# Performance work log

Hardware: AMD Instinct MI355X
Metric: run time of the kernel (lower is better)

The kernel has to match this reference:

```python
import jax, jax.numpy as jnp
import numpy as np

LN_EPS = 1e-5
NEG_SLOPE = 0.01  # torch LeakyReLU default


def layernorm(x, w, b):
    m = jnp.mean(x, axis=-1, keepdims=True)
    v = jnp.mean((x - m) ** 2, axis=-1, keepdims=True)
    return (x - m) * jax.lax.rsqrt(v + LN_EPS) * w + b


def setup_inputs() -> dict:
    key = jax.random.key(0)
    ks = jax.random.split(key, 12)
    B, T, C, E = 16, 1024, 768, 2
    d = C
    s = 0.02
    inp = {
        "x": jax.random.normal(ks[0], (B, T, C), jnp.float32),
        "ln1_w": jnp.ones((C,), jnp.float32),
        "ln1_b": jnp.zeros((C,), jnp.float32),
        "wqkv": jax.random.normal(ks[1], (C, 3 * C), jnp.float32) * s,
        "bqkv": jnp.zeros((3 * C,), jnp.float32),
        "wproj": jax.random.normal(ks[2], (C, C), jnp.float32) * s,
        "bproj": jnp.zeros((C,), jnp.float32),
        "ln2_w": jnp.ones((C,), jnp.float32),
        "ln2_b": jnp.zeros((C,), jnp.float32),
        "wg": jax.random.normal(ks[3], (C, E), jnp.float32) * s,
        # Experts module uses torch.randn (std 1); we scale down for numerics
        "w1": jax.random.normal(ks[4], (E, d, 4 * d), jnp.float32) * s,
        "w2": jax.random.normal(ks[5], (E, 4 * d, 4 * d), jnp.float32) * s,
        "w3": jax.random.normal(ks[6], (E, 4 * d, d), jnp.float32) * s,
        "n_head": 12,
    }
    return inp


def block_forward(x, ln1_w, ln1_b, wqkv, bqkv, wproj, bproj,
                  ln2_w, ln2_b, wg, w1, w2, w3, n_head):
    B, T, C = x.shape
    H = n_head
    hd = C // H
    E = wg.shape[-1]

    # ---- causal self-attention + residual ----
    h = layernorm(x, ln1_w, ln1_b)
    qkv = h @ wqkv + bqkv                      # [B,T,3C]
    q, k, v = jnp.split(qkv, 3, axis=-1)
    q = q.reshape(B, T, H, hd).transpose(0, 2, 1, 3)  # bhtd
    k = k.reshape(B, T, H, hd).transpose(0, 2, 1, 3)
    v = v.reshape(B, T, H, hd).transpose(0, 2, 1, 3)
    scores = jnp.einsum('bhqd,bhkd->bhqk', q, k) / jnp.sqrt(jnp.float32(hd))
    causal = jnp.tril(jnp.ones((T, T), bool))
    scores = jnp.where(causal, scores, jnp.finfo(scores.dtype).min)
    attn = jax.nn.softmax(scores, axis=-1)
    y = jnp.einsum('bhqk,bhkd->bhqd', attn, v)
    y = y.transpose(0, 2, 1, 3).reshape(B, T, C)
    x = x + (y @ wproj + bproj)

    # ---- MoE (top-2 gating, capacity dispatch) + residual ----
    h2 = layernorm(x, ln2_w, ln2_b)
    capacity = (T * 2) // E                    # capacity_factor = 1.0, top-2
    raw_gates = jax.nn.softmax(h2 @ wg, axis=-1)   # [B,T,E]

    idx1 = jnp.argmax(raw_gates, axis=-1)
    mask1 = jax.nn.one_hot(idx1, E, dtype=raw_gates.dtype)
    gate1 = jnp.sum(raw_gates * mask1, axis=-1)    # [B,T]
    gates2 = raw_gates * (1.0 - mask1)
    idx2 = jnp.argmax(gates2, axis=-1)
    mask2 = jax.nn.one_hot(idx2, E, dtype=raw_gates.dtype)
    gate2 = jnp.sum(raw_gates * mask2, axis=-1)
    denom = gate1 + gate2 + 1e-9
    gate1, gate2 = gate1 / denom, gate2 / denom

    # aux load-balancing loss (before capacity truncation)
    density = jnp.mean(mask1, axis=1)              # [B,E]
    density_proxy = jnp.mean(raw_gates, axis=1)    # [B,E]
    aux_loss = jnp.mean(density * density_proxy) * (E * E)

    # positions within each expert buffer (exclusive cumsum over tokens)
    pos1 = jnp.cumsum(mask1, axis=1) - mask1       # [B,T,E]
    mask1 = mask1 * (pos1 < capacity)
    mask1_count = jnp.sum(mask1, axis=1, keepdims=True)
    pos2 = (jnp.cumsum(mask2, axis=1) - mask2) + mask1_count
    mask2 = mask2 * (pos2 < capacity)

    oh1 = jax.nn.one_hot(pos1.astype(jnp.int32), capacity, dtype=raw_gates.dtype)
    oh2 = jax.nn.one_hot(pos2.astype(jnp.int32), capacity, dtype=raw_gates.dtype)
    combine = (gate1[..., None] * mask1)[..., None] * oh1 \
            + (gate2[..., None] * mask2)[..., None] * oh2   # [B,T,E,C]
    dispatch = (combine > 0).astype(h2.dtype)

    # dispatch -> per-expert batches
    expert_in = jnp.einsum('bnd,bnec->ebcd', h2, dispatch)   # [E,B,Cap,d]
    Bc = B * capacity
    ei = expert_in.reshape(E, Bc, C)
    lrelu = lambda z: jnp.where(z >= 0, z, NEG_SLOPE * z)
    hh = lrelu(jnp.einsum('end,edh->enh', ei, w1))
    hh = lrelu(jnp.einsum('end,edh->enh', hh, w2))
    eo = jnp.einsum('end,edh->enh', hh, w3).reshape(E, B, capacity, C)
    moe_out = jnp.einsum('ebcd,bnec->bnd', eo, combine)

    x = x + moe_out
    return x, aux_loss


def reference(x, ln1_w, ln1_b, wqkv, bqkv, wproj, bproj,
              ln2_w, ln2_b, wg, w1, w2, w3, n_head):
    return block_forward(x, ln1_w, ln1_b, wqkv, bqkv, wproj, bproj,
                         ln2_w, ln2_b, wg, w1, w2, w3, n_head)
```

## Files before the change

### kernel.cpp

```cpp
#include <hip/hip_runtime.h>
#include <cstdint>
#include <cstddef>

constexpr int B_  = 16;
constexpr int T_  = 1024;
constexpr int C_  = 768;
constexpr int H_  = 12;
constexpr int HD_ = 64;
constexpr int BT_ = B_ * T_;
constexpr int C3_ = 3 * C_;
constexpr int FF_ = 4 * C_;
constexpr int MCH_ = 8192;

typedef __bf16 bf16x8 __attribute__((ext_vector_type(8)));
typedef float  floatx4 __attribute__((ext_vector_type(4)));
typedef unsigned short u16x8 __attribute__((ext_vector_type(8)));

__device__ inline float bf2f(unsigned short u) {
  union { unsigned int i; float f; } x; x.i = ((unsigned int)u) << 16; return x.f;
}
__device__ inline unsigned short f2bf(float f) {
  union { float f; unsigned int i; } x; x.f = f;
  unsigned int u = x.i;
  u += 0x7fffu + ((u >> 16) & 1u);
  return (unsigned short)(u >> 16);
}

#define GLOAD_LDS16(gp, lp)                                              \
  __builtin_amdgcn_global_load_lds(                                      \
      (__attribute__((address_space(1))) void*)(gp),                     \
      (__attribute__((address_space(3))) void*)(lp), 16, 0, 0)

__launch_bounds__(256)
__global__ void ln_kernel(const float* __restrict__ x, const float* __restrict__ w,
                          const float* __restrict__ b, unsigned short* __restrict__ out) {
  int row = blockIdx.x;
  int tid = threadIdx.x;
  const float* xr = x + (size_t)row * C_;
  float v0 = xr[tid], v1 = xr[tid + 256], v2 = xr[tid + 512];
  float s  = v0 + v1 + v2;
  float ss = v0 * v0 + v1 * v1 + v2 * v2;
#pragma unroll
  for (int off = 32; off > 0; off >>= 1) {
    s  += __shfl_down(s, off, 64);
    ss += __shfl_down(ss, off, 64);
  }
  __shared__ float red[8];
  int wid = tid >> 6;
  if ((tid & 63) == 0) { red[wid] = s; red[4 + wid] = ss; }
  __syncthreads();
  float st  = red[0] + red[1] + red[2] + red[3];
  float sst = red[4] + red[5] + red[6] + red[7];
  float mean = st * (1.0f / C_);
  float var  = sst * (1.0f / C_) - mean * mean;
  float rstd = rsqrtf(var + 1e-5f);
  unsigned short* orow = out + (size_t)row * C_;
  orow[tid]       = f2bf((v0 - mean) * rstd * w[tid]       + b[tid]);
  orow[tid + 256] = f2bf((v1 - mean) * rstd * w[tid + 256] + b[tid + 256]);
  orow[tid + 512] = f2bf((v2 - mean) * rstd * w[tid + 512] + b[tid + 512]);
}

__launch_bounds__(256)
__global__ void convT(const float* __restrict__ in, unsigned short* __restrict__ out,
                      int K, int N) {
  __shared__ float t[32][33];
  int n0 = blockIdx.x * 32, k0 = blockIdx.y * 32;
  int tx = threadIdx.x & 31, ty = threadIdx.x >> 5;
#pragma unroll
  for (int r = 0; r < 32; r += 8)
    t[r + ty][tx] = in[(size_t)(k0 + r + ty) * N + n0 + tx];
  __syncthreads();
#pragma unroll
  for (int r = 0; r < 32; r += 8)
    out[(size_t)(n0 + r + ty) * K + k0 + tx] = f2bf(t[tx][r + ty]);
}

template <int ACT, bool BIAS, bool RES, bool COMBINE, bool OUTBF16>
__launch_bounds__(256)
__global__ void gemm_bf16(const unsigned short* __restrict__ A,
                          const unsigned short* __restrict__ Bt,
                          const float* __restrict__ bias,
                          const float* __restrict__ Rres,
                          const float* __restrict__ gates2, int eidx,
                          void* __restrict__ Cout,
                          int M, int N, int K) {
  __shared__ __attribute__((aligned(16))) unsigned short Als[8192];
  __shared__ __attribute__((aligned(16))) unsigned short Bls[8192];
  const int tid  = threadIdx.x;
  const int wave = tid >> 6, lane = tid & 63;
  const int wr = wave >> 1, wc = wave & 1;
  const int m0 = blockIdx.y * 128, n0 = blockIdx.x * 128;

  const int srow = wave * 32 + (lane >> 3);
  const int skg  = (lane & 7) ^ ((lane >> 3) & 7);
  const unsigned short* Ap = A  + (size_t)(m0 + srow) * K + skg * 8;
  const unsigned short* Bp = Bt + (size_t)(n0 + srow) * K + skg * 8;
  unsigned short* AlsW = Als + wave * 2048;
  unsigned short* BlsW = Bls + wave * 2048;

  floatx4 acc[4][4];
#pragma unroll
  for (int i = 0; i < 4; ++i)
#pragma unroll
    for (int j = 0; j < 4; ++j) acc[i][j] = floatx4{0.f, 0.f, 0.f, 0.f};

  const int q  = lane >> 4;
  const int ml = lane & 15;
  const int rsw = ml & 7;

  for (int k0 = 0; k0 < K; k0 += 64) {
    __syncthreads();
#pragma unroll
    for (int i = 0; i < 4; ++i) {
      GLOAD_LDS16(Ap + (size_t)(i * 8) * K + k0, AlsW + i * 512);
      GLOAD_LDS16(Bp + (size_t)(i * 8) * K + k0, BlsW + i * 512);
    }
    __syncthreads();
#pragma unroll
    for (int ks = 0; ks < 2; ++ks) {
      const int p = (ks * 4 + q) ^ rsw;
      bf16x8 af[4], bfg[4];
#pragma unroll
      for (int i = 0; i < 4; ++i) {
        int ar = wr * 64 + i * 16 + ml;
        af[i]  = *(const bf16x8*)&Als[(ar * 8 + p) * 8];
        int br = wc * 64 + i * 16 + ml;
        bfg[i] = *(const bf16x8*)&Bls[(br * 8 + p) * 8];
      }
#pragma unroll
      for (int i = 0; i < 4; ++i)
#pragma unroll
        for (int j = 0; j < 4; ++j)
          acc[i][j] = __builtin_amdgcn_mfma_f32_16x16x32_bf16(af[i], bfg[j], acc[i][j], 0, 0, 0);
    }
  }

  const int rbase = q * 4;
#pragma unroll
  for (int i = 0; i < 4; ++i) {
    int row = m0 + wr * 64 + i * 16 + rbase;
#pragma unroll
    for (int j = 0; j < 4; ++j) {
      int col = n0 + wc * 64 + j * 16 + ml;
      float bcol = BIAS ? bias[col] : 0.f;
#pragma unroll
      for (int r = 0; r < 4; ++r) {
        float v = acc[i][j][r];
        if (BIAS) v += bcol;
        if (ACT == 1) v = (v >= 0.f) ? v : 0.01f * v;
        if (RES) v += Rres[(size_t)(row + r) * N + col];
        if (COMBINE) {
          float g = gates2[2 * (row + r) + eidx];
          float* op = (float*)Cout + (size_t)(row + r) * N + col;
          *op += g * v;
        } else if (OUTBF16) {
          ((unsigned short*)Cout)[(size_t)(row + r) * N + col] = f2bf(v);
        } else {
          ((float*)Cout)[(size_t)(row + r) * N + col] = v;
        }
      }
    }
  }
}

#define GB256_BAR()   asm volatile("s_barrier" ::: "memory")
#define GB256_LGKM0() asm volatile("s_waitcnt lgkmcnt(0)" ::: "memory")

template <int ACT, bool BIAS>
__launch_bounds__(512, 2)
__global__ void gemm256(const unsigned short* __restrict__ A,
                        const unsigned short* __restrict__ Bt,
                        const float* __restrict__ bias,
                        unsigned short* __restrict__ Cout,
                        int M, int N, int K) {
  __shared__ __attribute__((aligned(16))) unsigned short L[65536];
  const int tid = threadIdx.x;
  const int w = tid >> 6, l = tid & 63;
  const int wr = w >> 2, wc = w & 3;
  const int ml = l & 15, q = l >> 4;
  const int m0 = blockIdx.y * 256, n0 = blockIdx.x * 256;

  const int srow = l >> 2;
  const int sg   = ((l & 3) ^ ((l >> 3) & 3)) * 8;
  const unsigned short* Ast = A  + (size_t)(m0 + srow) * K + sg;
  const unsigned short* Bst = Bt + (size_t)(n0 + srow) * K + sg;
  const int ldsw = w * 1024;

#define STG(cb, mat, ks, srcp, kk)                                           \
  do {                                                                       \
    const unsigned short* _s = (srcp) + (size_t)(w * 32) * K + (kk) + (ks) * 32; \
    unsigned short* _d = L + (cb) * 32768 + (mat) * 16384 + (ks) * 8192 + ldsw;  \
    GLOAD_LDS16(_s, _d);                                                     \
    GLOAD_LDS16(_s + (size_t)16 * K, _d + 512);                              \
  } while (0)

  const int dphys = (q ^ ((ml >> 1) & 3)) * 8;
  const int aoff = (wr * 128 + ml) * 32 + dphys;
  const int boff = (wc * 64 + ml) * 32 + dphys;

  floatx4 acc[8][4];
#pragma unroll
  for (int m = 0; m < 8; ++m)
#pragma unroll
    for (int n = 0; n < 4; ++n) acc[m][n] = floatx4{0.f, 0.f, 0.f, 0.f};

  const int NT = K >> 6;

  STG(0, 0, 0, Ast, 0);  STG(0, 1, 0, Bst, 0);
  STG(0, 0, 1, Ast, 0);  STG(0, 1, 1, Bst, 0);
  STG(1, 0, 0, Ast, 64); STG(1, 1, 0, Bst, 64);
  asm volatile("s_waitcnt vmcnt(0)" ::: "memory");
  GB256_BAR();

  for (int j = 0; j < NT; ++j) {
    const int c = j & 1, nx = c ^ 1;
    const int kk1 = (j + 1) << 6, kk2 = (j + 2) << 6;
    const bool st1 = (j + 1 < NT), st2 = (j + 2 < NT);
    bf16x8 bA[4], bB[4];

#define LOAD_A(KS, MH)                                                       \
  _Pragma("unroll")                                                          \
  for (int mq = 0; mq < 4; ++mq)                                             \
    bA[mq] = *(const bf16x8*)&L[c * 32768 + (KS) * 8192 + aoff + ((MH) * 4 + mq) * 512];
#define LOAD_B(KS)                                                           \
  _Pragma("unroll")                                                          \
  for (int n = 0; n < 4; ++n)                                                \
    bB[n] = *(const bf16x8*)&L[c * 32768 + 16384 + (KS) * 8192 + boff + n * 512];
#define MFMA16(MH)                                                           \
  __builtin_amdgcn_s_setprio(1);                                             \
  _Pragma("unroll")                                                          \
  for (int mq = 0; mq < 4; ++mq)                                             \
    _Pragma("unroll")                                                        \
    for (int n = 0; n < 4; ++n)                                              \
      acc[(MH) * 4 + mq][n] = __builtin_amdgcn_mfma_f32_16x16x32_bf16(       \
          bA[mq], bB[n], acc[(MH) * 4 + mq][n], 0, 0, 0);                    \
  __builtin_amdgcn_s_setprio(0);

    LOAD_B(0); LOAD_A(0, 0);
    if (st1) STG(nx, 0, 1, Ast, kk1);
    GB256_BAR(); GB256_LGKM0();
    MFMA16(0);
    GB256_BAR();

    LOAD_A(0, 1);
    if (st1) STG(nx, 1, 1, Bst, kk1);
    GB256_BAR(); GB256_LGKM0();
    MFMA16(1);
    GB256_BAR();

    LOAD_B(1); LOAD_A(1, 0);
    if (st2) STG(c, 0, 0, Ast, kk2);
    GB256_BAR(); GB256_LGKM0();
    MFMA16(0);
    GB256_BAR();

    LOAD_A(1, 1);
    if (st2) STG(c, 1, 0, Bst, kk2);
    GB256_BAR(); GB256_LGKM0();
    MFMA16(1);
    if (st2)      asm volatile("s_waitcnt vmcnt(4)" ::: "memory");
    else if (st1) asm volatile("s_waitcnt vmcnt(0)" ::: "memory");
    GB256_BAR();
#undef LOAD_A
#undef LOAD_B
#undef MFMA16
  }

#pragma unroll
  for (int m = 0; m < 8; ++m) {
    const int row = m0 + wr * 128 + m * 16 + q * 4;
#pragma unroll
    for (int n = 0; n < 4; ++n) {
      const int col = n0 + wc * 64 + n * 16 + ml;
      const float bcol = BIAS ? bias[col] : 0.f;
#pragma unroll
      for (int r = 0; r < 4; ++r) {
        float v = acc[m][n][r];
        if (BIAS) v += bcol;
        if (ACT == 1) v = (v >= 0.f) ? v : 0.01f * v;
        Cout[(size_t)(row + r) * N + col] = f2bf(v);
      }
    }
  }
#undef STG
}

__launch_bounds__(256)
__global__ void attn_kernel(const unsigned short* __restrict__ qkv,
                            unsigned short* __restrict__ y) {
  __shared__ __attribute__((aligned(16))) unsigned short Qls[64 * 64];
  __shared__ __attribute__((aligned(16))) unsigned short Kls[64 * 64];
  __shared__ __attribute__((aligned(16))) unsigned short Vt[64 * 72];
  __shared__ __attribute__((aligned(16))) unsigned short Pls[4 * 16 * 72];

  const int tid  = threadIdx.x;
  const int wave = tid >> 6, lane = tid & 63;
  const int quad = lane >> 4, n = lane & 15;
  const int q0 = blockIdx.x * 64;
  const int bh = blockIdx.y;
  const int b = bh / H_, h = bh % H_;
  const size_t base = (size_t)b * T_ * C3_ + (size_t)h * HD_;

  {
    const int r8 = lane >> 3;
    const int g  = (lane & 7) ^ r8;
#pragma unroll
    for (int i = 0; i < 2; ++i) {
      int row = wave * 16 + i * 8 + r8;
      GLOAD_LDS16(qkv + base + (size_t)(q0 + row) * C3_ + g * 8,
                  Qls + wave * 1024 + i * 512);
    }
  }

  floatx4 O[4];
#pragma unroll
  for (int ct = 0; ct < 4; ++ct) O[ct] = floatx4{0.f, 0.f, 0.f, 0.f};
  float mrow[4] = {-1e30f, -1e30f, -1e30f, -1e30f};
  float lrow[4] = {0.f, 0.f, 0.f, 0.f};

  const int nkt = blockIdx.x + 1;
  unsigned short* Pw = Pls + wave * (16 * 72);

  for (int kt = 0; kt < nkt; ++kt) {
    const int k0 = kt << 6;
    __syncthreads();
    {
      const int r8 = lane >> 3;
      const int g  = (lane & 7) ^ r8;
#pragma unroll
      for (int i = 0; i < 2; ++i) {
        int key = wave * 16 + i * 8 + r8;
        GLOAD_LDS16(qkv + base + (size_t)(k0 + key) * C3_ + C_ + g * 8,
                    Kls + wave * 1024 + i * 512);
      }
    }
    {
      int key = tid & 63;
      int dbase = (tid >> 6) * 8;
#pragma unroll
      for (int it = 0; it < 2; ++it) {
        int d0 = dbase + it * 32;
        u16x8 vv = *(const u16x8*)(qkv + base + (size_t)(k0 + key) * C3_ + 2 * C_ + d0);
#pragma unroll
        for (int j = 0; j < 8; ++j) Vt[(d0 + j) * 72 + key] = vv[j];
      }
    }
    __syncthreads();

    floatx4 sacc[4];
#pragma unroll
    for (int ct = 0; ct < 4; ++ct) sacc[ct] = floatx4{0.f, 0.f, 0.f, 0.f};
#pragma unroll
    for (int ks = 0; ks < 2; ++ks) {
      const int ga = (ks * 4 + quad) ^ (n & 7);
      bf16x8 aq = *(const bf16x8*)&Qls[((wave * 16 + n) * 8 + ga) * 8];
#pragma unroll
      for (int ct = 0; ct < 4; ++ct) {
        bf16x8 kb = *(const bf16x8*)&Kls[((ct * 16 + n) * 8 + ga) * 8];
        sacc[ct] = __builtin_amdgcn_mfma_f32_16x16x32_bf16(aq, kb, sacc[ct], 0, 0, 0);
      }
    }

    float p[4][4];
#pragma unroll
    for (int ct = 0; ct < 4; ++ct)
#pragma unroll
      for (int r = 0; r < 4; ++r) p[ct][r] = sacc[ct][r] * 0.125f;
    if (kt == nkt - 1) {
      const int kgb = k0 + n, qgb = q0 + wave * 16 + quad * 4;
#pragma unroll
      for (int ct = 0; ct < 4; ++ct)
#pragma unroll
        for (int r = 0; r < 4; ++r)
          if (kgb + ct * 16 > qgb + r) p[ct][r] = -1e30f;
    }
#pragma unroll
    for (int r = 0; r < 4; ++r) {
      float tm = fmaxf(fmaxf(p[0][r], p[1][r]), fmaxf(p[2][r], p[3][r]));
      tm = fmaxf(tm, __shfl_xor(tm, 1, 64));
      tm = fmaxf(tm, __shfl_xor(tm, 2, 64));
      tm = fmaxf(tm, __shfl_xor(tm, 4, 64));
      tm = fmaxf(tm, __shfl_xor(tm, 8, 64));
      float mn = fmaxf(mrow[r], tm);
      float alpha = __expf(mrow[r] - mn);
      mrow[r] = mn;
      float ps = 0.f;
#pragma unroll
      for (int ct = 0; ct < 4; ++ct) {
        float pe = __expf(p[ct][r] - mn);
        p[ct][r] = pe;
        ps += pe;
      }
      ps += __shfl_xor(ps, 1, 64);
      ps += __shfl_xor(ps, 2, 64);
      ps += __shfl_xor(ps, 4, 64);
      ps += __shfl_xor(ps, 8, 64);
      lrow[r] = lrow[r] * alpha + ps;
      O[0][r] *= alpha; O[1][r] *= alpha; O[2][r] *= alpha; O[3][r] *= alpha;
    }

#pragma unroll
    for (int ct = 0; ct < 4; ++ct)
#pragma unroll
      for (int r = 0; r < 4; ++r)
        Pw[(quad * 4 + r) * 72 + ct * 16 + n] = f2bf(p[ct][r]);

#pragma unroll
    for (int ks = 0; ks < 2; ++ks) {
      bf16x8 pa = *(const bf16x8*)&Pw[n * 72 + (ks * 4 + quad) * 8];
#pragma unroll
      for (int ct = 0; ct < 4; ++ct) {
        bf16x8 vb = *(const bf16x8*)&Vt[(ct * 16 + n) * 72 + (ks * 4 + quad) * 8];
        O[ct] = __builtin_amdgcn_mfma_f32_16x16x32_bf16(pa, vb, O[ct], 0, 0, 0);
      }
    }
  }

#pragma unroll
  for (int r = 0; r < 4; ++r) {
    float inv = 1.0f / lrow[r];
    int row = q0 + wave * 16 + quad * 4 + r;
    unsigned short* dst = y + ((size_t)b * T_ + row) * C_ + h * HD_;
#pragma unroll
    for (int ct = 0; ct < 4; ++ct)
      dst[ct * 16 + n] = f2bf(O[ct][r] * inv);
  }
}

__launch_bounds__(256)
__global__ void gate_kernel(const unsigned short* __restrict__ h2,
                            const float* __restrict__ wg,
                            float* __restrict__ gates) {
  int wave = threadIdx.x >> 6, lane = threadIdx.x & 63;
  int t = blockIdx.x * 4 + wave;
  const unsigned short* hr = h2 + (size_t)t * C_;
  float a0 = 0.0f, a1 = 0.0f;
#pragma unroll
  for (int i = 0; i < 12; ++i) {
    int d = lane + 64 * i;
    float hv = bf2f(hr[d]);
    a0 += hv * wg[2 * d];
    a1 += hv * wg[2 * d + 1];
  }
#pragma unroll
  for (int off = 32; off > 0; off >>= 1) {
    a0 += __shfl_down(a0, off, 64);
    a1 += __shfl_down(a1, off, 64);
  }
  if (lane == 0) {
    float m  = fmaxf(a0, a1);
    float e0 = __expf(a0 - m), e1 = __expf(a1 - m);
    float invs = 1.0f / (e0 + e1);
    float p0 = e0 * invs, p1 = e1 * invs;
    const float gnorm = 1.0f / (1.0f + 1e-9f);
    gates[2 * t]     = p0 * gnorm;
    gates[2 * t + 1] = p1 * gnorm;
  }
}

__launch_bounds__(1024)
__global__ void moe_stats_kernel(const float* __restrict__ gates,
                                 float* __restrict__ out_aux) {
  int wave = threadIdx.x >> 6, lane = threadIdx.x & 63;
  float c0 = 0.f, sp0 = 0.f, sp1 = 0.f;
#pragma unroll
  for (int j = 0; j < 16; ++j) {
    int t = wave * T_ + lane + 64 * j;
    float p0 = gates[2 * t], p1 = gates[2 * t + 1];
    c0  += (p1 > p0) ? 0.f : 1.f;
    sp0 += p0;
    sp1 += p1;
  }
#pragma unroll
  for (int off = 32; off > 0; off >>= 1) {
    c0  += __shfl_down(c0, off, 64);
    sp0 += __shfl_down(sp0, off, 64);
    sp1 += __shfl_down(sp1, off, 64);
  }
  __shared__ float red[16][3];
  if (lane == 0) { red[wave][0] = c0; red[wave][1] = sp0; red[wave][2] = sp1; }
  __syncthreads();
  if (threadIdx.x == 0) {
    float s = 0.f;
    for (int b = 0; b < B_; ++b) {
      float cc0 = red[b][0];
      float d0 = cc0 * (1.f / T_), d1 = (T_ - cc0) * (1.f / T_);
      float px0 = red[b][1] * (1.f / T_), px1 = red[b][2] * (1.f / T_);
      s += d0 * px0 + d1 * px1;
    }
    out_aux[0] = s * (4.f / 32.f);
  }
}

extern "C" void kernel_launch(void* const* d_in, const int* in_sizes, int n_in,
                              void* d_out, int out_size, void* d_ws, size_t ws_size,
                              hipStream_t stream) {
  const float* x     = (const float*)d_in[0];
  const float* ln1_w = (const float*)d_in[1];
  const float* ln1_b = (const float*)d_in[2];
  const float* wqkv  = (const float*)d_in[3];
  const float* bqkv  = (const float*)d_in[4];
  const float* wproj = (const float*)d_in[5];
  const float* bproj = (const float*)d_in[6];
  const float* ln2_w = (const float*)d_in[7];
  const float* ln2_b = (const float*)d_in[8];
  const float* wg    = (const float*)d_in[9];
  const float* w1    = (const float*)d_in[10];
  const float* w2    = (const float*)d_in[11];
  const float* w3    = (const float*)d_in[12];
  float* out = (float*)d_out;

  unsigned short* wsu   = (unsigned short*)d_ws;
  unsigned short* wqkvT = wsu;
  unsigned short* wprojT= wqkvT + (size_t)C3_ * C_;
  unsigned short* w1T   = wprojT + (size_t)C_ * C_;
  unsigned short* w2T   = w1T + (size_t)2 * FF_ * C_;
  unsigned short* w3T   = w2T + (size_t)2 * FF_ * FF_;
  unsigned short* hb    = w3T + (size_t)2 * C_ * FF_;
  unsigned short* region= hb + (size_t)BT_ * C_;
  unsigned short* qkvb  = region;
  unsigned short* yb    = region + (size_t)BT_ * C3_;
  unsigned short* hh1   = region;
  unsigned short* hh2   = region + (size_t)MCH_ * FF_;
  float* gates = (float*)(region + (size_t)BT_ * 4 * C_);

  convT<<<dim3(C3_ / 32, C_ / 32), 256, 0, stream>>>(wqkv, wqkvT, C_, C3_);
  convT<<<dim3(C_ / 32, C_ / 32), 256, 0, stream>>>(wproj, wprojT, C_, C_);
  for (int e = 0; e < 2; ++e) {
    convT<<<dim3(FF_ / 32, C_ / 32), 256, 0, stream>>>(
        w1 + (size_t)e * C_ * FF_, w1T + (size_t)e * FF_ * C_, C_, FF_);
    convT<<<dim3(FF_ / 32, FF_ / 32), 256, 0, stream>>>(
        w2 + (size_t)e * FF_ * FF_, w2T + (size_t)e * FF_ * FF_, FF_, FF_);
    convT<<<dim3(C_ / 32, FF_ / 32), 256, 0, stream>>>(
        w3 + (size_t)e * FF_ * C_, w3T + (size_t)e * C_ * FF_, FF_, C_);
  }

  ln_kernel<<<BT_, 256, 0, stream>>>(x, ln1_w, ln1_b, hb);
  gemm256<0, true><<<dim3(C3_ / 256, BT_ / 256), 512, 0, stream>>>(
      hb, wqkvT, bqkv, qkvb, BT_, C3_, C_);
  attn_kernel<<<dim3(T_ / 64, B_ * H_), 256, 0, stream>>>(qkvb, yb);
  gemm_bf16<0, true, true, false, false><<<dim3(C_ / 128, BT_ / 128), 256, 0, stream>>>(
      yb, wprojT, bproj, x, nullptr, 0, out, BT_, C_, C_);

  ln_kernel<<<BT_, 256, 0, stream>>>(out, ln2_w, ln2_b, hb);
  gate_kernel<<<BT_ / 4, 256, 0, stream>>>(hb, wg, gates);
  moe_stats_kernel<<<1, 1024, 0, stream>>>(gates, out + (size_t)BT_ * C_);

  for (int e = 0; e < 2; ++e) {
    for (int c = 0; c < BT_ / MCH_; ++c) {
      const unsigned short* a = hb + (size_t)c * MCH_ * C_;
      gemm256<1, false><<<dim3(FF_ / 256, MCH_ / 256), 512, 0, stream>>>(
          a, w1T + (size_t)e * FF_ * C_, nullptr, hh1, MCH_, FF_, C_);
      gemm256<1, false><<<dim3(FF_ / 256, MCH_ / 256), 512, 0, stream>>>(
          hh1, w2T + (size_t)e * FF_ * FF_, nullptr, hh2, MCH_, FF_, FF_);
      gemm_bf16<0, false, false, true, false><<<dim3(C_ / 128, MCH_ / 128), 256, 0, stream>>>(
          hh2, w3T + (size_t)e * C_ * FF_, nullptr, nullptr,
          gates + (size_t)2 * c * MCH_, e, out + (size_t)c * MCH_ * C_, MCH_, C_, FF_);
    }
  }
}
```

Baseline: 1.820 ms.

## Emit transposed V from QKV GEMM and double-buffer K/V loads in attention

The QKV projection now runs on the 128-tile GEMM with a split epilogue that writes Q/K row-major and V transposed into a separate buffer. Attention can then load V with async global-to-LDS copies instead of a per-element register transpose, and K/V tiles are double-buffered so the next tile's load overlaps current compute. The W1 expert GEMM also switches from the 256-tile to the 128-tile kernel. Risks include uncoalesced strided writes for the transposed V, lower GEMM efficiency with smaller tiles, and a missing barrier between the async LDS load and its use.

```diff
diff --git a/kernel.cpp b/kernel.cpp
--- a/kernel.cpp
+++ b/kernel.cpp
@@ -9,6 +9,7 @@
 constexpr int HD_ = 64;
 constexpr int BT_ = B_ * T_;
 constexpr int C3_ = 3 * C_;
+constexpr int QK2_ = 2 * C_;
 constexpr int FF_ = 4 * C_;
 constexpr int MCH_ = 8192;
 
@@ -75,7 +76,7 @@
     out[(size_t)(n0 + r + ty) * K + k0 + tx] = f2bf(t[tx][r + ty]);
 }
 
-template <int ACT, bool BIAS, bool RES, bool COMBINE, bool OUTBF16>
+template <int ACT, bool BIAS, bool RES, bool COMBINE, bool OUTBF16, bool VSPLIT = false>
 __launch_bounds__(256)
 __global__ void gemm_bf16(const unsigned short* __restrict__ A,
                           const unsigned short* __restrict__ Bt,
@@ -83,6 +84,7 @@
                           const float* __restrict__ Rres,
                           const float* __restrict__ gates2, int eidx,
                           void* __restrict__ Cout,
+                          unsigned short* __restrict__ vtout,
                           int M, int N, int K) {
   __shared__ __attribute__((aligned(16))) unsigned short Als[8192];
   __shared__ __attribute__((aligned(16))) unsigned short Bls[8192];
@@ -153,6 +155,12 @@
           float g = gates2[2 * (row + r) + eidx];
           float* op = (float*)Cout + (size_t)(row + r) * N + col;
           *op += g * v;
+        } else if (VSPLIT) {
+          if (col < QK2_) {
+            ((unsigned short*)Cout)[(size_t)(row + r) * QK2_ + col] = f2bf(v);
+          } else {
+            vtout[(size_t)(col - QK2_) * BT_ + row + r] = f2bf(v);
+          }
         } else if (OUTBF16) {
           ((unsigned short*)Cout)[(size_t)(row + r) * N + col] = f2bf(v);
         } else {
@@ -286,11 +294,12 @@
 }
 
 __launch_bounds__(256)
-__global__ void attn_kernel(const unsigned short* __restrict__ qkv,
+__global__ void attn_kernel(const unsigned short* __restrict__ qk,
+                            const unsigned short* __restrict__ vT,
                             unsigned short* __restrict__ y) {
   __shared__ __attribute__((aligned(16))) unsigned short Qls[64 * 64];
-  __shared__ __attribute__((aligned(16))) unsigned short Kls[64 * 64];
-  __shared__ __attribute__((aligned(16))) unsigned short Vt[64 * 72];
+  __shared__ __attribute__((aligned(16))) unsigned short K2[2][64 * 64];
+  __shared__ __attribute__((aligned(16))) unsigned short V2[2][64 * 64];
   __shared__ __attribute__((aligned(16))) unsigned short Pls[4 * 16 * 72];
 
   const int tid  = threadIdx.x;
@@ -299,18 +308,32 @@
   const int q0 = blockIdx.x * 64;
   const int bh = blockIdx.y;
   const int b = bh / H_, h = bh % H_;
-  const size_t base = (size_t)b * T_ * C3_ + (size_t)h * HD_;
-
-  {
-    const int r8 = lane >> 3;
-    const int g  = (lane & 7) ^ r8;
-#pragma unroll
-    for (int i = 0; i < 2; ++i) {
-      int row = wave * 16 + i * 8 + r8;
-      GLOAD_LDS16(qkv + base + (size_t)(q0 + row) * C3_ + g * 8,
-                  Qls + wave * 1024 + i * 512);
-    }
-  }
+  const size_t qbase = (size_t)b * T_ * QK2_ + (size_t)h * HD_;
+  const size_t vbase = (size_t)h * HD_ * BT_ + (size_t)b * T_;
+
+  const int r8 = lane >> 3;
+  const int g  = (lane & 7) ^ r8;
+
+#pragma unroll
+  for (int i = 0; i < 2; ++i) {
+    int row = wave * 16 + i * 8 + r8;
+    GLOAD_LDS16(qk + qbase + (size_t)(q0 + row) * QK2_ + g * 8,
+                Qls + wave * 1024 + i * 512);
+  }
+
+#define STAGE_KV(bf, k0)                                                      \
+  do {                                                                        \
+    _Pragma("unroll")                                                         \
+    for (int i = 0; i < 2; ++i) {                                             \
+      int row = wave * 16 + i * 8 + r8;                                       \
+      GLOAD_LDS16(qk + qbase + (size_t)((k0) + row) * QK2_ + C_ + g * 8,      \
+                  K2[bf] + wave * 1024 + i * 512);                            \
+      GLOAD_LDS16(vT + vbase + (size_t)row * BT_ + (k0) + g * 8,              \
+                  V2[bf] + wave * 1024 + i * 512);                            \
+    }                                                                         \
+  } while (0)
+
+  STAGE_KV(0, 0);
 
   floatx4 O[4];
 #pragma unroll
@@ -322,30 +345,9 @@
   unsigned short* Pw = Pls + wave * (16 * 72);
 
   for (int kt = 0; kt < nkt; ++kt) {
-    const int k0 = kt << 6;
+    const int cur = kt & 1;
     __syncthreads();
-    {
-      const int r8 = lane >> 3;
-      const int g  = (lane & 7) ^ r8;
-#pragma unroll
-      for (int i = 0; i < 2; ++i) {
-        int key = wave * 16 + i * 8 + r8;
-        GLOAD_LDS16(qkv + base + (size_t)(k0 + key) * C3_ + C_ + g * 8,
-                    Kls + wave * 1024 + i * 512);
-      }
-    }
-    {
-      int key = tid & 63;
-      int dbase = (tid >> 6) * 8;
-#pragma unroll
-      for (int it = 0; it < 2; ++it) {
-        int d0 = dbase + it * 32;
-        u16x8 vv = *(const u16x8*)(qkv + base + (size_t)(k0 + key) * C3_ + 2 * C_ + d0);
-#pragma unroll
-        for (int j = 0; j < 8; ++j) Vt[(d0 + j) * 72 + key] = vv[j];
-      }
-    }
-    __syncthreads();
+    if (kt + 1 < nkt) STAGE_KV(cur ^ 1, (kt + 1) << 6);
 
     floatx4 sacc[4];
 #pragma unroll
@@ -356,7 +358,7 @@
       bf16x8 aq = *(const bf16x8*)&Qls[((wave * 16 + n) * 8 + ga) * 8];
 #pragma unroll
       for (int ct = 0; ct < 4; ++ct) {
-        bf16x8 kb = *(const bf16x8*)&Kls[((ct * 16 + n) * 8 + ga) * 8];
+        bf16x8 kb = *(const bf16x8*)&K2[cur][((ct * 16 + n) * 8 + ga) * 8];
         sacc[ct] = __builtin_amdgcn_mfma_f32_16x16x32_bf16(aq, kb, sacc[ct], 0, 0, 0);
       }
     }
@@ -367,7 +369,7 @@
 #pragma unroll
       for (int r = 0; r < 4; ++r) p[ct][r] = sacc[ct][r] * 0.125f;
     if (kt == nkt - 1) {
-      const int kgb = k0 + n, qgb = q0 + wave * 16 + quad * 4;
+      const int kgb = (kt << 6) + n, qgb = q0 + wave * 16 + quad * 4;
 #pragma unroll
       for (int ct = 0; ct < 4; ++ct)
 #pragma unroll
@@ -408,9 +410,10 @@
 #pragma unroll
     for (int ks = 0; ks < 2; ++ks) {
       bf16x8 pa = *(const bf16x8*)&Pw[n * 72 + (ks * 4 + quad) * 8];
+      const int gv = (ks * 4 + quad) ^ (n & 7);
 #pragma unroll
       for (int ct = 0; ct < 4; ++ct) {
-        bf16x8 vb = *(const bf16x8*)&Vt[(ct * 16 + n) * 72 + (ks * 4 + quad) * 8];
+        bf16x8 vb = *(const bf16x8*)&V2[cur][((ct * 16 + n) * 8 + gv) * 8];
         O[ct] = __builtin_amdgcn_mfma_f32_16x16x32_bf16(pa, vb, O[ct], 0, 0, 0);
       }
     }
@@ -425,6 +428,7 @@
     for (int ct = 0; ct < 4; ++ct)
       dst[ct * 16 + n] = f2bf(O[ct][r] * inv);
   }
+#undef STAGE_KV
 }
 
 __launch_bounds__(256)
@@ -518,8 +522,9 @@
   unsigned short* w3T   = w2T + (size_t)2 * FF_ * FF_;
   unsigned short* hb    = w3T + (size_t)2 * C_ * FF_;
   unsigned short* region= hb + (size_t)BT_ * C_;
-  unsigned short* qkvb  = region;
-  unsigned short* yb    = region + (size_t)BT_ * C3_;
+  unsigned short* qkb   = region;
+  unsigned short* vTb   = region + (size_t)BT_ * QK2_;
+  unsigned short* yb    = region + (size_t)BT_ * 3 * C_;
   unsigned short* hh1   = region;
   unsigned short* hh2   = region + (size_t)MCH_ * FF_;
   float* gates = (float*)(region + (size_t)BT_ * 4 * C_);
@@ -536,11 +541,11 @@
   }
 
   ln_kernel<<<BT_, 256, 0, stream>>>(x, ln1_w, ln1_b, hb);
-  gemm256<0, true><<<dim3(C3_ / 256, BT_ / 256), 512, 0, stream>>>(
-      hb, wqkvT, bqkv, qkvb, BT_, C3_, C_);
-  attn_kernel<<<dim3(T_ / 64, B_ * H_), 256, 0, stream>>>(qkvb, yb);
+  gemm_bf16<0, true, false, false, true, true><<<dim3(C3_ / 128, BT_ / 128), 256, 0, stream>>>(
+      hb, wqkvT, bqkv, nullptr, nullptr, 0, qkb, vTb, BT_, C3_, C_);
+  attn_kernel<<<dim3(T_ / 64, B_ * H_), 256, 0, stream>>>(qkb, vTb, yb);
   gemm_bf16<0, true, true, false, false><<<dim3(C_ / 128, BT_ / 128), 256, 0, stream>>>(
-      yb, wprojT, bproj, x, nullptr, 0, out, BT_, C_, C_);
+      yb, wprojT, bproj, x, nullptr, 0, out, nullptr, BT_, C_, C_);
 
   ln_kernel<<<BT_, 256, 0, stream>>>(out, ln2_w, ln2_b, hb);
   gate_kernel<<<BT_ / 4, 256, 0, stream>>>(hb, wg, gates);
@@ -549,13 +554,13 @@
   for (int e = 0; e < 2; ++e) {
     for (int c = 0; c < BT_ / MCH_; ++c) {
       const unsigned short* a = hb + (size_t)c * MCH_ * C_;
-      gemm256<1, false><<<dim3(FF_ / 256, MCH_ / 256), 512, 0, stream>>>(
-          a, w1T + (size_t)e * FF_ * C_, nullptr, hh1, MCH_, FF_, C_);
+      gemm_bf16<1, false, false, false, true><<<dim3(FF_ / 128, MCH_ / 128), 256, 0, stream>>>(
+          a, w1T + (size_t)e * FF_ * C_, nullptr, nullptr, nullptr, 0, hh1, nullptr, MCH_, FF_, C_);
       gemm256<1, false><<<dim3(FF_ / 256, MCH_ / 256), 512, 0, stream>>>(
           hh1, w2T + (size_t)e * FF_ * FF_, nullptr, hh2, MCH_, FF_, FF_);
       gemm_bf16<0, false, false, true, false><<<dim3(C_ / 128, MCH_ / 128), 256, 0, stream>>>(
           hh2, w3T + (size_t)e * C_ * FF_, nullptr, nullptr,
-          gates + (size_t)2 * c * MCH_, e, out + (size_t)c * MCH_ * C_, MCH_, C_, FF_);
-    }
-  }
-}
+          gates + (size_t)2 * c * MCH_, e, out + (size_t)c * MCH_ * C_, nullptr, MCH_, C_, FF_);
+    }
+  }
+}
```

New measurement: 1.811 ms. No clear change (-0.5%).
